# Performance work log

Hardware: AMD Instinct MI355X
Metric: run time of the kernel (lower is better)

Reference implementation:

```python
import jax, jax.numpy as jnp
import numpy as np

N_NODES = 100000
N_EDGES = 1600000
IN_DIM = 64
HID = 128
N_ASSETS = 50
N_GRAPHS = 64


def setup_inputs() -> dict:
    key = jax.random.key(0)
    ks = jax.random.split(key, 12)
    x = jax.random.normal(ks[0], (N_NODES, IN_DIM), dtype=jnp.float32)
    edge_index = jax.random.randint(ks[1], (2, N_EDGES), 0, N_NODES, dtype=jnp.int64)
    batch = jnp.sort(jax.random.randint(ks[2], (N_NODES,), 0, N_GRAPHS, dtype=jnp.int64))
    def lin(k, fan_in, fan_out):
        bound = 1.0 / np.sqrt(fan_in)
        return jax.random.uniform(k, (fan_in, fan_out), jnp.float32, -bound, bound)
    return {
        "x": x,
        "edge_index": edge_index,
        "batch": batch,
        # GraphConv 1: lin_rel (with bias) on aggregated messages, lin_root (no bias)
        "w1_rel": lin(ks[3], IN_DIM, HID),
        "b1": jnp.zeros((HID,), jnp.float32),
        "w1_root": lin(ks[4], IN_DIM, HID),
        # GraphConv 2
        "w2_rel": lin(ks[5], HID, HID),
        "b2": jnp.zeros((HID,), jnp.float32),
        "w2_root": lin(ks[6], HID, HID),
        # MLP head
        "fc1_w": lin(ks[7], HID, HID),
        "fc1_b": jnp.zeros((HID,), jnp.float32),
        "fc2_w": lin(ks[8], HID, N_ASSETS),
        "fc2_b": jnp.zeros((N_ASSETS,), jnp.float32),
    }


def graph_conv(x, src, dst, w_rel, w_root, b):
    # out_i = W_rel @ (sum_{j: j->i} x_j) + W_root @ x_i + b  (PyG GraphConv, aggr='add')
    # Project first (cheaper traffic when out_dim <= in_dim is not guaranteed, but
    # aggregating raw features then projecting matches math; project-then-scatter is
    # equivalent by linearity and lets the scatter run at out width. Keep faithful
    # order: aggregate raw x_j, then lin_rel.
    agg = jax.ops.segment_sum(x[src], dst, num_segments=N_NODES)  # [N, in_dim]
    return agg @ w_rel + x @ w_root + b


def reference(x, edge_index, batch, w1_rel, b1, w1_root, w2_rel, b2, w2_root,
              fc1_w, fc1_b, fc2_w, fc2_b):
    src, dst = edge_index[0], edge_index[1]
    h = jax.nn.relu(graph_conv(x, src, dst, w1_rel, w1_root, b1))   # [N, HID]
    h = jax.nn.relu(graph_conv(h, src, dst, w2_rel, w2_root, b2))   # [N, HID]
    # global_mean_pool over batch segment ids
    sums = jax.ops.segment_sum(h, batch, num_segments=N_GRAPHS)     # [G, HID]
    cnts = jax.ops.segment_sum(jnp.ones((h.shape[0], 1), h.dtype), batch,
                               num_segments=N_GRAPHS)               # [G, 1]
    pooled = sums / jnp.maximum(cnts, 1.0)
    out = jax.nn.relu(pooled @ fc1_w + fc1_b)
    logits = out @ fc2_w + fc2_b
    return jax.nn.softmax(logits, axis=-1)
```

## Files before the change

### kernel.cpp

```cpp
#include <hip/hip_runtime.h>
#include <math.h>

#define N_NODES_C 100000
#define N_EDGES_C 1600000
#define IN_DIM_C 64
#define HID_C 128
#define N_ASSETS_C 50
#define N_GRAPHS_C 64

#define BKT_SHIFT 9
#define BKT_NODES 512
#define NB_BKT ((N_NODES_C + BKT_NODES - 1) / BKT_NODES)
#define EPB_A 8192
#define NBLK_A ((N_EDGES_C + EPB_A - 1) / EPB_A)

typedef __attribute__((ext_vector_type(8))) short bf16x8;
typedef __attribute__((ext_vector_type(4))) float f32x4;

__device__ __forceinline__ unsigned short f2bf(float f) {
    unsigned u = __float_as_uint(f);
    return (unsigned short)((u + 0x7FFFu + ((u >> 16) & 1u)) >> 16);
}
__device__ __forceinline__ float bf2f(unsigned short b) {
    return __uint_as_float((unsigned)b << 16);
}
__device__ __forceinline__ void acc_bf8(float* acc, uint4 v) {
    acc[0] += __uint_as_float(v.x << 16);
    acc[1] += __uint_as_float(v.x & 0xFFFF0000u);
    acc[2] += __uint_as_float(v.y << 16);
    acc[3] += __uint_as_float(v.y & 0xFFFF0000u);
    acc[4] += __uint_as_float(v.z << 16);
    acc[5] += __uint_as_float(v.z & 0xFFFF0000u);
    acc[6] += __uint_as_float(v.w << 16);
    acc[7] += __uint_as_float(v.w & 0xFFFF0000u);
}

__global__ __launch_bounds__(256) void cast_bf16_kernel(
    const float* __restrict__ src, unsigned short* __restrict__ dst, int n4)
{
    int i = blockIdx.x * 256 + threadIdx.x;
    if (i < n4) {
        float4 v = ((const float4*)src)[i];
        ushort4 o;
        o.x = f2bf(v.x); o.y = f2bf(v.y); o.z = f2bf(v.z); o.w = f2bf(v.w);
        ((ushort4*)dst)[i] = o;
    }
}

__global__ __launch_bounds__(64) void pack_w_kernel(
    const float* __restrict__ W, unsigned short* __restrict__ dst)
{
    int kc = blockIdx.x >> 3;
    int ct = blockIdx.x & 7;
    int lane = threadIdx.x;
    int quad = lane >> 4;
    int l16 = lane & 15;
    unsigned short hi[8], lo[8];
#pragma unroll
    for (int j = 0; j < 8; ++j) {
        float w = W[(size_t)(kc * 32 + quad * 8 + j) * HID_C + ct * 16 + l16];
        unsigned short h = f2bf(w);
        float r = w - bf2f(h);
        hi[j] = h;
        lo[j] = f2bf(r);
    }
    size_t base = ((size_t)(kc * 8 + ct) * 2) * 512 + (size_t)lane * 8;
#pragma unroll
    for (int j = 0; j < 8; ++j) {
        dst[base + j] = hi[j];
        dst[base + 512 + j] = lo[j];
    }
}

__global__ __launch_bounds__(256) void bucket_hist_kernel(
    const int* __restrict__ ei, int* __restrict__ bcnt)
{
    __shared__ int cnt[NB_BKT];
    int t = threadIdx.x;
    for (int i = t; i < NB_BKT; i += 256) cnt[i] = 0;
    __syncthreads();
    int base = blockIdx.x * 2048;
#pragma unroll
    for (int i = 0; i < 8; ++i) {
        int e = base + i * 256 + t;
        if (e < N_EDGES_C) {
            int dst = ei[N_EDGES_C + e];
            atomicAdd(&cnt[dst >> BKT_SHIFT], 1);
        }
    }
    __syncthreads();
    for (int i = t; i < NB_BKT; i += 256)
        if (cnt[i]) atomicAdd(&bcnt[i], cnt[i]);
}

__global__ __launch_bounds__(256) void bucket_scan_kernel(
    const int* __restrict__ bcnt, int* __restrict__ bbase, int* __restrict__ gcur)
{
    __shared__ int s[256];
    int t = threadIdx.x;
    int v = (t < NB_BKT) ? bcnt[t] : 0;
    s[t] = v;
    __syncthreads();
    for (int o = 1; o < 256; o <<= 1) {
        int x = (t >= o) ? s[t - o] : 0;
        __syncthreads();
        s[t] += x;
        __syncthreads();
    }
    int excl = s[t] - v;
    if (t < NB_BKT) { bbase[t] = excl; gcur[t] = excl; }
    if (t == 255) bbase[NB_BKT] = s[255];
}

__global__ __launch_bounds__(256) void partition_kernel(
    const int* __restrict__ ei, int* __restrict__ gcur,
    unsigned* __restrict__ tmp)
{
    __shared__ unsigned stage[EPB_A];
    __shared__ unsigned stage2[EPB_A];
    __shared__ unsigned char sbkt[EPB_A];
    __shared__ unsigned char sbkt2[EPB_A];
    __shared__ int cnt[NB_BKT];
    __shared__ int base[NB_BKT];
    __shared__ int cur[NB_BKT];
    __shared__ int gb[NB_BKT];
    __shared__ int s[256];

    const int t = threadIdx.x;
    const int e0 = blockIdx.x * EPB_A;
    const int nE = min(EPB_A, N_EDGES_C - e0);

    for (int i = t; i < NB_BKT; i += 256) cnt[i] = 0;
    __syncthreads();

    for (int idx = t; idx < nE; idx += 256) {
        int e = e0 + idx;
        int src = ei[e];
        int dst = ei[N_EDGES_C + e];
        int b = dst >> BKT_SHIFT;
        stage[idx] = ((unsigned)(dst & (BKT_NODES - 1)) << 17) | (unsigned)src;
        sbkt[idx] = (unsigned char)b;
        atomicAdd(&cnt[b], 1);
    }
    __syncthreads();

    int v = (t < NB_BKT) ? cnt[t] : 0;
    s[t] = v;
    __syncthreads();
    for (int o = 1; o < 256; o <<= 1) {
        int x = (t >= o) ? s[t - o] : 0;
        __syncthreads();
        s[t] += x;
        __syncthreads();
    }
    if (t < NB_BKT) {
        int excl = s[t] - v;
        base[t] = excl;
        cur[t] = excl;
        gb[t] = atomicAdd(&gcur[t], v);
    }
    __syncthreads();

    for (int idx = t; idx < nE; idx += 256) {
        int b = sbkt[idx];
        int p = atomicAdd(&cur[b], 1);
        stage2[p] = stage[idx];
        sbkt2[p] = (unsigned char)b;
    }
    __syncthreads();

    for (int idx = t; idx < nE; idx += 256) {
        int b = sbkt2[idx];
        int dest = gb[b] + (idx - base[b]);
        tmp[dest] = stage2[idx];
    }
}

__global__ __launch_bounds__(256) void bucket_sort_kernel(
    const unsigned* __restrict__ tmp, const int* __restrict__ bbase,
    int* __restrict__ row_ptr, int* __restrict__ col)
{
    __shared__ int ldeg[BKT_NODES];
    __shared__ int lsum[256];
    const int t = threadIdx.x;
    const int b = blockIdx.x;
    const int beg = bbase[b];
    const int end = bbase[b + 1];

    ldeg[t] = 0; ldeg[t + 256] = 0;
    __syncthreads();

    for (int p = beg + t; p < end; p += 256)
        atomicAdd(&ldeg[tmp[p] >> 17], 1);
    __syncthreads();

    int a0 = ldeg[2 * t], a1 = ldeg[2 * t + 1];
    int pair = a0 + a1;
    lsum[t] = pair;
    __syncthreads();
    for (int o = 1; o < 256; o <<= 1) {
        int x = (t >= o) ? lsum[t - o] : 0;
        __syncthreads();
        lsum[t] += x;
        __syncthreads();
    }
    int ep = lsum[t] - pair;
    __syncthreads();
    ldeg[2 * t] = ep;
    ldeg[2 * t + 1] = ep + a0;

    int gn0 = b * BKT_NODES + 2 * t;
    if (gn0 < N_NODES_C)     row_ptr[gn0] = beg + ep;
    if (gn0 + 1 < N_NODES_C) row_ptr[gn0 + 1] = beg + ep + a0;
    if (b == NB_BKT - 1 && t == 0) row_ptr[N_NODES_C] = N_EDGES_C;
    __syncthreads();

    for (int p = beg + t; p < end; p += 256) {
        unsigned v = tmp[p];
        int pos = atomicAdd(&ldeg[v >> 17], 1);
        col[beg + pos] = (int)(v & 0x1FFFFu);
    }
}

__global__ __launch_bounds__(256) void gather_bf128_kernel(
    const unsigned short* __restrict__ feat, const int* __restrict__ row_ptr,
    const int* __restrict__ col, unsigned short* __restrict__ agg)
{
    int wave = threadIdx.x >> 6;
    int lane = threadIdx.x & 63;
    int g = lane >> 4;
    int c = lane & 15;
    int n = blockIdx.x * 4 + wave;
    if (n >= N_NODES_C) return;
    int beg = row_ptr[n], end = row_ptr[n + 1];
    const uint4* f4 = (const uint4*)feat;

    float acc[8];
#pragma unroll
    for (int j = 0; j < 8; ++j) acc[j] = 0.f;

    int e = beg + g;
    for (; e + 12 < end; e += 16) {
        int s0 = col[e], s1 = col[e + 4], s2 = col[e + 8], s3 = col[e + 12];
        uint4 v0 = f4[(size_t)s0 * 16 + c];
        uint4 v1 = f4[(size_t)s1 * 16 + c];
        uint4 v2 = f4[(size_t)s2 * 16 + c];
        uint4 v3 = f4[(size_t)s3 * 16 + c];
        acc_bf8(acc, v0); acc_bf8(acc, v1); acc_bf8(acc, v2); acc_bf8(acc, v3);
    }
    if (e + 4 < end) {
        int s0 = col[e], s1 = col[e + 4];
        uint4 v0 = f4[(size_t)s0 * 16 + c];
        uint4 v1 = f4[(size_t)s1 * 16 + c];
        acc_bf8(acc, v0); acc_bf8(acc, v1);
        e += 8;
    }
    if (e < end) {
        uint4 v = f4[(size_t)col[e] * 16 + c];
        acc_bf8(acc, v);
    }
#pragma unroll
    for (int j = 0; j < 8; ++j) {
        acc[j] += __shfl_xor(acc[j], 16, 64);
        acc[j] += __shfl_xor(acc[j], 32, 64);
    }
    if (g == 0) {
        uint4 o;
        o.x = (unsigned)f2bf(acc[0]) | ((unsigned)f2bf(acc[1]) << 16);
        o.y = (unsigned)f2bf(acc[2]) | ((unsigned)f2bf(acc[3]) << 16);
        o.z = (unsigned)f2bf(acc[4]) | ((unsigned)f2bf(acc[5]) << 16);
        o.w = (unsigned)f2bf(acc[6]) | ((unsigned)f2bf(acc[7]) << 16);
        ((uint4*)agg)[(size_t)n * 16 + c] = o;
    }
}

__global__ __launch_bounds__(256) void gather_bf64_kernel(
    const unsigned short* __restrict__ feat, const int* __restrict__ row_ptr,
    const int* __restrict__ col, unsigned short* __restrict__ agg)
{
    int wave = threadIdx.x >> 6;
    int lane = threadIdx.x & 63;
    int g = lane >> 3;
    int c = lane & 7;
    int n = blockIdx.x * 4 + wave;
    if (n >= N_NODES_C) return;
    int beg = row_ptr[n], end = row_ptr[n + 1];
    const uint4* f4 = (const uint4*)feat;

    float acc[8];
#pragma unroll
    for (int j = 0; j < 8; ++j) acc[j] = 0.f;

    int e = beg + g;
    for (; e + 8 < end; e += 16) {
        int s0 = col[e], s1 = col[e + 8];
        uint4 v0 = f4[(size_t)s0 * 8 + c];
        uint4 v1 = f4[(size_t)s1 * 8 + c];
        acc_bf8(acc, v0); acc_bf8(acc, v1);
    }
    if (e < end) {
        uint4 v = f4[(size_t)col[e] * 8 + c];
        acc_bf8(acc, v);
    }
#pragma unroll
    for (int j = 0; j < 8; ++j) {
        acc[j] += __shfl_xor(acc[j], 8, 64);
        acc[j] += __shfl_xor(acc[j], 16, 64);
        acc[j] += __shfl_xor(acc[j], 32, 64);
    }
    if (g == 0) {
        uint4 o;
        o.x = (unsigned)f2bf(acc[0]) | ((unsigned)f2bf(acc[1]) << 16);
        o.y = (unsigned)f2bf(acc[2]) | ((unsigned)f2bf(acc[3]) << 16);
        o.z = (unsigned)f2bf(acc[4]) | ((unsigned)f2bf(acc[5]) << 16);
        o.w = (unsigned)f2bf(acc[6]) | ((unsigned)f2bf(acc[7]) << 16);
        ((uint4*)agg)[(size_t)n * 8 + c] = o;
    }
}

template<int K>
__device__ __forceinline__ void conv_phase(
    const unsigned short* __restrict__ P, const unsigned short* __restrict__ WP,
    const int* rowIdx, int quad, int lane, int wv, f32x4 acc[4][2])
{
#pragma unroll
    for (int kc = 0; kc < K / 32; ++kc) {
        bf16x8 afr[4];
#pragma unroll
        for (int rt = 0; rt < 4; ++rt)
            afr[rt] = *(const bf16x8*)(P + (size_t)rowIdx[rt] * K + kc * 32 + quad * 8);
#pragma unroll
        for (int ci = 0; ci < 2; ++ci) {
            int ct = wv * 2 + ci;
            const unsigned short* bp = WP + ((size_t)(kc * 8 + ct) * 2) * 512 + (size_t)lane * 8;
            bf16x8 bhi = *(const bf16x8*)bp;
            bf16x8 blo = *(const bf16x8*)(bp + 512);
#pragma unroll
            for (int rt = 0; rt < 4; ++rt) {
                acc[rt][ci] = __builtin_amdgcn_mfma_f32_16x16x32_bf16(afr[rt], bhi, acc[rt][ci], 0, 0, 0);
                acc[rt][ci] = __builtin_amdgcn_mfma_f32_16x16x32_bf16(afr[rt], blo, acc[rt][ci], 0, 0, 0);
            }
        }
    }
}

template<int KA, int KX>
__global__ __launch_bounds__(256) void conv_mfma_kernel(
    const unsigned short* __restrict__ A, const unsigned short* __restrict__ X,
    const unsigned short* __restrict__ WrP, const unsigned short* __restrict__ WoP,
    const float* __restrict__ bias, unsigned short* __restrict__ outp, int N)
{
    const int t = threadIdx.x;
    const int wv = t >> 6;
    const int lane = t & 63;
    const int quad = lane >> 4;
    const int l16 = lane & 15;
    const int n0 = blockIdx.x * 64;

    f32x4 acc[4][2];
#pragma unroll
    for (int rt = 0; rt < 4; ++rt)
#pragma unroll
        for (int ci = 0; ci < 2; ++ci)
            acc[rt][ci] = (f32x4){0.f, 0.f, 0.f, 0.f};

    int rowIdx[4];
#pragma unroll
    for (int rt = 0; rt < 4; ++rt) {
        int r = n0 + rt * 16 + l16;
        rowIdx[rt] = (r < N) ? r : (N - 1);
    }

    conv_phase<KA>(A, WrP, rowIdx, quad, lane, wv, acc);
    conv_phase<KX>(X, WoP, rowIdx, quad, lane, wv, acc);

#pragma unroll
    for (int ci = 0; ci < 2; ++ci) {
        int colg = wv * 32 + ci * 16 + l16;
        float bv = bias[colg];
#pragma unroll
        for (int rt = 0; rt < 4; ++rt) {
            int nbase = n0 + rt * 16 + quad * 4;
#pragma unroll
            for (int r = 0; r < 4; ++r) {
                int node = nbase + r;
                if (node < N)
                    outp[(size_t)node * HID_C + colg] = f2bf(fmaxf(acc[rt][ci][r] + bv, 0.f));
            }
        }
    }
}

template<int KA, int KX>
__global__ __launch_bounds__(256) void conv_mfma_pool_kernel(
    const unsigned short* __restrict__ A, const unsigned short* __restrict__ X,
    const unsigned short* __restrict__ WrP, const unsigned short* __restrict__ WoP,
    const float* __restrict__ bias, const int* __restrict__ batch,
    float* __restrict__ pooled, int N)
{
    __shared__ int sbatch[64];
    const int t = threadIdx.x;
    const int wv = t >> 6;
    const int lane = t & 63;
    const int quad = lane >> 4;
    const int l16 = lane & 15;
    const int n0 = blockIdx.x * 64;

    if (t < 64) {
        int node = n0 + t;
        sbatch[t] = (node < N) ? batch[node] : -1;
    }

    f32x4 acc[4][2];
#pragma unroll
    for (int rt = 0; rt < 4; ++rt)
#pragma unroll
        for (int ci = 0; ci < 2; ++ci)
            acc[rt][ci] = (f32x4){0.f, 0.f, 0.f, 0.f};

    int rowIdx[4];
#pragma unroll
    for (int rt = 0; rt < 4; ++rt) {
        int r = n0 + rt * 16 + l16;
        rowIdx[rt] = (r < N) ? r : (N - 1);
    }

    conv_phase<KA>(A, WrP, rowIdx, quad, lane, wv, acc);
    conv_phase<KX>(X, WoP, rowIdx, quad, lane, wv, acc);
    __syncthreads();

#pragma unroll
    for (int ci = 0; ci < 2; ++ci) {
        float bv = bias[wv * 32 + ci * 16 + l16];
#pragma unroll
        for (int rt = 0; rt < 4; ++rt)
#pragma unroll
            for (int r = 0; r < 4; ++r)
                acc[rt][ci][r] = fmaxf(acc[rt][ci][r] + bv, 0.f);
    }

    int gmin = sbatch[0];
    int gmax = batch[min(n0 + 63, N - 1)];
    for (int gg = gmin; gg <= gmax; ++gg) {
#pragma unroll
        for (int ci = 0; ci < 2; ++ci) {
            float p = 0.f;
#pragma unroll
            for (int rt = 0; rt < 4; ++rt) {
                int lbase = rt * 16 + quad * 4;
#pragma unroll
                for (int r = 0; r < 4; ++r)
                    if (sbatch[lbase + r] == gg) p += acc[rt][ci][r];
            }
            p += __shfl_xor(p, 16, 64);
            p += __shfl_xor(p, 32, 64);
            if (quad == 0)
                atomicAdd(&pooled[gg * HID_C + wv * 32 + ci * 16 + l16], p);
        }
    }
}

__global__ __launch_bounds__(256) void count_kernel(
    const int* __restrict__ batch, float* __restrict__ cnts, int N)
{
    __shared__ int h[N_GRAPHS_C];
    int t = threadIdx.x;
    if (t < N_GRAPHS_C) h[t] = 0;
    __syncthreads();
    int base = (blockIdx.x * 256 + t) * 16;
    int cur = -1, c = 0;
    for (int i = 0; i < 16; ++i) {
        int n = base + i;
        if (n < N) {
            int g = batch[n];
            if (g != cur) {
                if (cur >= 0) atomicAdd(&h[cur], c);
                cur = g; c = 0;
            }
            ++c;
        }
    }
    if (cur >= 0) atomicAdd(&h[cur], c);
    __syncthreads();
    if (t < N_GRAPHS_C && h[t]) atomicAdd(&cnts[t], (float)h[t]);
}

__global__ __launch_bounds__(128) void head_kernel(
    const float* __restrict__ pooled, const float* __restrict__ cnts,
    const float* __restrict__ fc1w, const float* __restrict__ fc1b,
    const float* __restrict__ fc2w, const float* __restrict__ fc2b,
    float* __restrict__ out)
{
    __shared__ float sp[HID_C];
    __shared__ float so[HID_C];
    __shared__ float sl[64];
    __shared__ float sred[2];
    int g = blockIdx.x;
    int j = threadIdx.x;

    float inv = 1.f / fmaxf(cnts[g], 1.f);
    sp[j] = pooled[g * HID_C + j] * inv;
    __syncthreads();

    float a = fc1b[j];
    for (int k = 0; k < HID_C; ++k) a = fmaf(sp[k], fc1w[k * HID_C + j], a);
    so[j] = fmaxf(a, 0.f);
    __syncthreads();

    if (j < N_ASSETS_C) {
        float l = fc2b[j];
        for (int k = 0; k < HID_C; ++k) l = fmaf(so[k], fc2w[k * N_ASSETS_C + j], l);
        sl[j] = l;
    }
    __syncthreads();

    if (j == 0) {
        float m = -1e30f;
        for (int q = 0; q < N_ASSETS_C; ++q) m = fmaxf(m, sl[q]);
        sred[0] = m;
    }
    __syncthreads();
    if (j < N_ASSETS_C) sl[j] = expf(sl[j] - sred[0]);
    __syncthreads();
    if (j == 0) {
        float s = 0.f;
        for (int q = 0; q < N_ASSETS_C; ++q) s += sl[q];
        sred[1] = 1.f / s;
    }
    __syncthreads();
    if (j < N_ASSETS_C) out[g * N_ASSETS_C + j] = sl[j] * sred[1];
}

extern "C" void kernel_launch(void* const* d_in, const int* in_sizes, int n_in,
                              void* d_out, int out_size, void* d_ws, size_t ws_size,
                              hipStream_t stream)
{
    const float* x       = (const float*)d_in[0];
    const int*   ei      = (const int*)d_in[1];
    const int*   batch   = (const int*)d_in[2];
    const float* w1_rel  = (const float*)d_in[3];
    const float* b1      = (const float*)d_in[4];
    const float* w1_root = (const float*)d_in[5];
    const float* w2_rel  = (const float*)d_in[6];
    const float* b2      = (const float*)d_in[7];
    const float* w2_root = (const float*)d_in[8];
    const float* fc1w    = (const float*)d_in[9];
    const float* fc1b    = (const float*)d_in[10];
    const float* fc2w    = (const float*)d_in[11];
    const float* fc2b    = (const float*)d_in[12];
    float* out = (float*)d_out;

    char* ws = (char*)d_ws;
    unsigned*       tmp     = (unsigned*)(ws + 0);
    int*            col     = (int*)(ws + 6400000);
    int*            row_ptr = (int*)(ws + 12800000);
    int*            bcnt    = (int*)(ws + 13200016);
    int*            bbase   = (int*)(ws + 13200816);
    int*            gcur    = (int*)(ws + 13201616);
    unsigned short* wp1r    = (unsigned short*)(ws + 13202432);
    unsigned short* wp1o    = (unsigned short*)(ws + 13235200);
    unsigned short* wp2r    = (unsigned short*)(ws + 13267968);
    unsigned short* wp2o    = (unsigned short*)(ws + 13333504);
    float*          pooled  = (float*)(ws + 13399040);
    float*          cnts    = (float*)(ws + 13431808);
    unsigned short* xb      = (unsigned short*)(ws + 13432064);
    unsigned short* agg1b   = (unsigned short*)(ws + 26232064);
    unsigned short* h1b     = (unsigned short*)(ws + 39032064);
    unsigned short* agg2b   = (unsigned short*)(ws + 64632064);

    hipMemsetAsync(pooled, 0, 33024, stream);
    hipMemsetAsync(bcnt, 0, 800, stream);

    cast_bf16_kernel<<<(N_NODES_C * IN_DIM_C / 4 + 255) / 256, 256, 0, stream>>>(x, xb, N_NODES_C * IN_DIM_C / 4);
    pack_w_kernel<<<(IN_DIM_C / 32) * 8, 64, 0, stream>>>(w1_rel,  wp1r);
    pack_w_kernel<<<(IN_DIM_C / 32) * 8, 64, 0, stream>>>(w1_root, wp1o);
    pack_w_kernel<<<(HID_C  / 32) * 8, 64, 0, stream>>>(w2_rel,  wp2r);
    pack_w_kernel<<<(HID_C  / 32) * 8, 64, 0, stream>>>(w2_root, wp2o);

    count_kernel<<<(N_NODES_C + 4095) / 4096, 256, 0, stream>>>(batch, cnts, N_NODES_C);

    bucket_hist_kernel<<<(N_EDGES_C + 2047) / 2048, 256, 0, stream>>>(ei, bcnt);
    bucket_scan_kernel<<<1, 256, 0, stream>>>(bcnt, bbase, gcur);
    partition_kernel<<<NBLK_A, 256, 0, stream>>>(ei, gcur, tmp);
    bucket_sort_kernel<<<NB_BKT, 256, 0, stream>>>(tmp, bbase, row_ptr, col);

    const int ggrid = (N_NODES_C + 3) / 4;
    const int cgrid = (N_NODES_C + 63) / 64;

    gather_bf64_kernel<<<ggrid, 256, 0, stream>>>(xb, row_ptr, col, agg1b);
    conv_mfma_kernel<IN_DIM_C, IN_DIM_C><<<cgrid, 256, 0, stream>>>(
        agg1b, xb, wp1r, wp1o, b1, h1b, N_NODES_C);

    gather_bf128_kernel<<<ggrid, 256, 0, stream>>>(h1b, row_ptr, col, agg2b);
    conv_mfma_pool_kernel<HID_C, HID_C><<<cgrid, 256, 0, stream>>>(
        agg2b, h1b, wp2r, wp2o, b2, batch, pooled, N_NODES_C);

    head_kernel<<<N_GRAPHS_C, 128, 0, stream>>>(pooled, cnts, fc1w, fc1b, fc2w, fc2b, out);
}
```

Before: 348.2 us.

## Fuse neighbor gather into conv MFMA kernels via LDS staging, merge weight packing

Each conv kernel now gathers and sums neighbor features for its 64-node tile straight into shared memory, and the MFMA stage reads the aggregate from LDS. This removes the separate gather kernels and the global round-trip of the aggregated buffers. The four weight-pack launches are merged into one, and the two memsets are folded into one by moving bcnt next to pooled. In exchange, the gather now has less parallelism: one block covers 64 nodes sequentially, with 16 nodes per wave and the 2-way unroll used for both widths. That may hide memory latency worse than the old one-wave-per-node kernels.

```diff
diff --git a/kernel.cpp b/kernel.cpp
--- a/kernel.cpp
+++ b/kernel.cpp
@@ -34,6 +34,14 @@
     acc[6] += __uint_as_float(v.w << 16);
     acc[7] += __uint_as_float(v.w & 0xFFFF0000u);
 }
+__device__ __forceinline__ uint4 pack_bf8(const float* acc) {
+    uint4 o;
+    o.x = (unsigned)f2bf(acc[0]) | ((unsigned)f2bf(acc[1]) << 16);
+    o.y = (unsigned)f2bf(acc[2]) | ((unsigned)f2bf(acc[3]) << 16);
+    o.z = (unsigned)f2bf(acc[4]) | ((unsigned)f2bf(acc[5]) << 16);
+    o.w = (unsigned)f2bf(acc[6]) | ((unsigned)f2bf(acc[7]) << 16);
+    return o;
+}
 
 __global__ __launch_bounds__(256) void cast_bf16_kernel(
     const float* __restrict__ src, unsigned short* __restrict__ dst, int n4)
@@ -47,12 +55,11 @@
     }
 }
 
-__global__ __launch_bounds__(64) void pack_w_kernel(
-    const float* __restrict__ W, unsigned short* __restrict__ dst)
-{
-    int kc = blockIdx.x >> 3;
-    int ct = blockIdx.x & 7;
-    int lane = threadIdx.x;
+__device__ __forceinline__ void pack_w_body(
+    const float* __restrict__ W, unsigned short* __restrict__ dst, int bid, int lane)
+{
+    int kc = bid >> 3;
+    int ct = bid & 7;
     int quad = lane >> 4;
     int l16 = lane & 15;
     unsigned short hi[8], lo[8];
@@ -70,6 +77,20 @@
         dst[base + j] = hi[j];
         dst[base + 512 + j] = lo[j];
     }
+}
+
+__global__ __launch_bounds__(64) void pack_all_kernel(
+    const float* __restrict__ w1r, const float* __restrict__ w1o,
+    const float* __restrict__ w2r, const float* __restrict__ w2o,
+    unsigned short* __restrict__ p1r, unsigned short* __restrict__ p1o,
+    unsigned short* __restrict__ p2r, unsigned short* __restrict__ p2o)
+{
+    int b = blockIdx.x;
+    int lane = threadIdx.x;
+    if (b < 16)       pack_w_body(w1r, p1r, b, lane);
+    else if (b < 32)  pack_w_body(w1o, p1o, b - 16, lane);
+    else if (b < 64)  pack_w_body(w2r, p2r, b - 32, lane);
+    else              pack_w_body(w2o, p2o, b - 64, lane);
 }
 
 __global__ __launch_bounds__(256) void bucket_hist_kernel(
@@ -222,104 +243,8 @@
     }
 }
 
-__global__ __launch_bounds__(256) void gather_bf128_kernel(
-    const unsigned short* __restrict__ feat, const int* __restrict__ row_ptr,
-    const int* __restrict__ col, unsigned short* __restrict__ agg)
-{
-    int wave = threadIdx.x >> 6;
-    int lane = threadIdx.x & 63;
-    int g = lane >> 4;
-    int c = lane & 15;
-    int n = blockIdx.x * 4 + wave;
-    if (n >= N_NODES_C) return;
-    int beg = row_ptr[n], end = row_ptr[n + 1];
-    const uint4* f4 = (const uint4*)feat;
-
-    float acc[8];
-#pragma unroll
-    for (int j = 0; j < 8; ++j) acc[j] = 0.f;
-
-    int e = beg + g;
-    for (; e + 12 < end; e += 16) {
-        int s0 = col[e], s1 = col[e + 4], s2 = col[e + 8], s3 = col[e + 12];
-        uint4 v0 = f4[(size_t)s0 * 16 + c];
-        uint4 v1 = f4[(size_t)s1 * 16 + c];
-        uint4 v2 = f4[(size_t)s2 * 16 + c];
-        uint4 v3 = f4[(size_t)s3 * 16 + c];
-        acc_bf8(acc, v0); acc_bf8(acc, v1); acc_bf8(acc, v2); acc_bf8(acc, v3);
-    }
-    if (e + 4 < end) {
-        int s0 = col[e], s1 = col[e + 4];
-        uint4 v0 = f4[(size_t)s0 * 16 + c];
-        uint4 v1 = f4[(size_t)s1 * 16 + c];
-        acc_bf8(acc, v0); acc_bf8(acc, v1);
-        e += 8;
-    }
-    if (e < end) {
-        uint4 v = f4[(size_t)col[e] * 16 + c];
-        acc_bf8(acc, v);
-    }
-#pragma unroll
-    for (int j = 0; j < 8; ++j) {
-        acc[j] += __shfl_xor(acc[j], 16, 64);
-        acc[j] += __shfl_xor(acc[j], 32, 64);
-    }
-    if (g == 0) {
-        uint4 o;
-        o.x = (unsigned)f2bf(acc[0]) | ((unsigned)f2bf(acc[1]) << 16);
-        o.y = (unsigned)f2bf(acc[2]) | ((unsigned)f2bf(acc[3]) << 16);
-        o.z = (unsigned)f2bf(acc[4]) | ((unsigned)f2bf(acc[5]) << 16);
-        o.w = (unsigned)f2bf(acc[6]) | ((unsigned)f2bf(acc[7]) << 16);
-        ((uint4*)agg)[(size_t)n * 16 + c] = o;
-    }
-}
-
-__global__ __launch_bounds__(256) void gather_bf64_kernel(
-    const unsigned short* __restrict__ feat, const int* __restrict__ row_ptr,
-    const int* __restrict__ col, unsigned short* __restrict__ agg)
-{
-    int wave = threadIdx.x >> 6;
-    int lane = threadIdx.x & 63;
-    int g = lane >> 3;
-    int c = lane & 7;
-    int n = blockIdx.x * 4 + wave;
-    if (n >= N_NODES_C) return;
-    int beg = row_ptr[n], end = row_ptr[n + 1];
-    const uint4* f4 = (const uint4*)feat;
-
-    float acc[8];
-#pragma unroll
-    for (int j = 0; j < 8; ++j) acc[j] = 0.f;
-
-    int e = beg + g;
-    for (; e + 8 < end; e += 16) {
-        int s0 = col[e], s1 = col[e + 8];
-        uint4 v0 = f4[(size_t)s0 * 8 + c];
-        uint4 v1 = f4[(size_t)s1 * 8 + c];
-        acc_bf8(acc, v0); acc_bf8(acc, v1);
-    }
-    if (e < end) {
-        uint4 v = f4[(size_t)col[e] * 8 + c];
-        acc_bf8(acc, v);
-    }
-#pragma unroll
-    for (int j = 0; j < 8; ++j) {
-        acc[j] += __shfl_xor(acc[j], 8, 64);
-        acc[j] += __shfl_xor(acc[j], 16, 64);
-        acc[j] += __shfl_xor(acc[j], 32, 64);
-    }
-    if (g == 0) {
-        uint4 o;
-        o.x = (unsigned)f2bf(acc[0]) | ((unsigned)f2bf(acc[1]) << 16);
-        o.y = (unsigned)f2bf(acc[2]) | ((unsigned)f2bf(acc[3]) << 16);
-        o.z = (unsigned)f2bf(acc[4]) | ((unsigned)f2bf(acc[5]) << 16);
-        o.w = (unsigned)f2bf(acc[6]) | ((unsigned)f2bf(acc[7]) << 16);
-        ((uint4*)agg)[(size_t)n * 8 + c] = o;
-    }
-}
-
 template<int K>
-__device__ __forceinline__ void conv_phase(
+__device__ __forceinline__ void conv_phase_g(
     const unsigned short* __restrict__ P, const unsigned short* __restrict__ WP,
     const int* rowIdx, int quad, int lane, int wv, f32x4 acc[4][2])
 {
@@ -344,12 +269,46 @@
     }
 }
 
-template<int KA, int KX>
-__global__ __launch_bounds__(256) void conv_mfma_kernel(
-    const unsigned short* __restrict__ A, const unsigned short* __restrict__ X,
+template<int K, int RS>
+__device__ __forceinline__ void conv_phase_lds(
+    const unsigned short* __restrict__ sA, const unsigned short* __restrict__ WP,
+    int quad, int lane, int wv, int l16, f32x4 acc[4][2])
+{
+#pragma unroll
+    for (int kc = 0; kc < K / 32; ++kc) {
+        bf16x8 afr[4];
+#pragma unroll
+        for (int rt = 0; rt < 4; ++rt)
+            afr[rt] = *(const bf16x8*)(sA + (size_t)(rt * 16 + l16) * RS + kc * 32 + quad * 8);
+#pragma unroll
+        for (int ci = 0; ci < 2; ++ci) {
+            int ct = wv * 2 + ci;
+            const unsigned short* bp = WP + ((size_t)(kc * 8 + ct) * 2) * 512 + (size_t)lane * 8;
+            bf16x8 bhi = *(const bf16x8*)bp;
+            bf16x8 blo = *(const bf16x8*)(bp + 512);
+#pragma unroll
+            for (int rt = 0; rt < 4; ++rt) {
+                acc[rt][ci] = __builtin_amdgcn_mfma_f32_16x16x32_bf16(afr[rt], bhi, acc[rt][ci], 0, 0, 0);
+                acc[rt][ci] = __builtin_amdgcn_mfma_f32_16x16x32_bf16(afr[rt], blo, acc[rt][ci], 0, 0, 0);
+            }
+        }
+    }
+}
+
+template<int K, bool POOL>
+__global__ __launch_bounds__(256) void fused_conv_kernel(
+    const unsigned short* __restrict__ feat, const unsigned short* __restrict__ X,
+    const int* __restrict__ row_ptr, const int* __restrict__ col,
     const unsigned short* __restrict__ WrP, const unsigned short* __restrict__ WoP,
-    const float* __restrict__ bias, unsigned short* __restrict__ outp, int N)
-{
+    const float* __restrict__ bias, const int* __restrict__ batch,
+    float* __restrict__ pooled, unsigned short* __restrict__ outp, int N)
+{
+    constexpr int RS = K + 8;
+    constexpr int SG = K / 8;
+    constexpr int NSG = 64 / SG;
+    __shared__ __align__(16) unsigned short sA[64 * RS];
+    __shared__ int sbatch[64];
+
     const int t = threadIdx.x;
     const int wv = t >> 6;
     const int lane = t & 63;
@@ -357,6 +316,46 @@
     const int l16 = lane & 15;
     const int n0 = blockIdx.x * 64;
 
+    if (POOL && t < 64) {
+        int node = n0 + t;
+        sbatch[t] = (node < N) ? batch[node] : -1;
+    }
+
+    {
+        const int sg = lane / SG;
+        const int c  = lane % SG;
+        const uint4* f4 = (const uint4*)feat;
+        for (int i = 0; i < 16; ++i) {
+            int ln = wv * 16 + i;
+            int n = n0 + ln;
+            int beg = 0, end = 0;
+            if (n < N) { beg = row_ptr[n]; end = row_ptr[n + 1]; }
+            float acc[8];
+#pragma unroll
+            for (int j = 0; j < 8; ++j) acc[j] = 0.f;
+            int e = beg + sg;
+            for (; e + NSG < end; e += 2 * NSG) {
+                int s0 = col[e], s1 = col[e + NSG];
+                uint4 v0 = f4[(size_t)s0 * SG + c];
+                uint4 v1 = f4[(size_t)s1 * SG + c];
+                acc_bf8(acc, v0); acc_bf8(acc, v1);
+            }
+            if (e < end) {
+                uint4 v = f4[(size_t)col[e] * SG + c];
+                acc_bf8(acc, v);
+            }
+#pragma unroll
+            for (int j = 0; j < 8; ++j) {
+                if (NSG >= 8) acc[j] += __shfl_xor(acc[j], 8, 64);
+                acc[j] += __shfl_xor(acc[j], 16, 64);
+                acc[j] += __shfl_xor(acc[j], 32, 64);
+            }
+            if (sg == 0)
+                *(uint4*)(sA + (size_t)ln * RS + c * 8) = pack_bf8(acc);
+        }
+    }
+    __syncthreads();
+
     f32x4 acc[4][2];
 #pragma unroll
     for (int rt = 0; rt < 4; ++rt)
@@ -371,91 +370,53 @@
         rowIdx[rt] = (r < N) ? r : (N - 1);
     }
 
-    conv_phase<KA>(A, WrP, rowIdx, quad, lane, wv, acc);
-    conv_phase<KX>(X, WoP, rowIdx, quad, lane, wv, acc);
-
-#pragma unroll
-    for (int ci = 0; ci < 2; ++ci) {
-        int colg = wv * 32 + ci * 16 + l16;
-        float bv = bias[colg];
-#pragma unroll
-        for (int rt = 0; rt < 4; ++rt) {
-            int nbase = n0 + rt * 16 + quad * 4;
-#pragma unroll
-            for (int r = 0; r < 4; ++r) {
-                int node = nbase + r;
-                if (node < N)
-                    outp[(size_t)node * HID_C + colg] = f2bf(fmaxf(acc[rt][ci][r] + bv, 0.f));
-            }
-        }
-    }
-}
-
-template<int KA, int KX>
-__global__ __launch_bounds__(256) void conv_mfma_pool_kernel(
-    const unsigned short* __restrict__ A, const unsigned short* __restrict__ X,
-    const unsigned short* __restrict__ WrP, const unsigned short* __restrict__ WoP,
-    const float* __restrict__ bias, const int* __restrict__ batch,
-    float* __restrict__ pooled, int N)
-{
-    __shared__ int sbatch[64];
-    const int t = threadIdx.x;
-    const int wv = t >> 6;
-    const int lane = t & 63;
-    const int quad = lane >> 4;
-    const int l16 = lane & 15;
-    const int n0 = blockIdx.x * 64;
-
-    if (t < 64) {
-        int node = n0 + t;
-        sbatch[t] = (node < N) ? batch[node] : -1;
-    }
-
-    f32x4 acc[4][2];
-#pragma unroll
-    for (int rt = 0; rt < 4; ++rt)
-#pragma unroll
-        for (int ci = 0; ci < 2; ++ci)
-            acc[rt][ci] = (f32x4){0.f, 0.f, 0.f, 0.f};
-
-    int rowIdx[4];
-#pragma unroll
-    for (int rt = 0; rt < 4; ++rt) {
-        int r = n0 + rt * 16 + l16;
-        rowIdx[rt] = (r < N) ? r : (N - 1);
-    }
-
-    conv_phase<KA>(A, WrP, rowIdx, quad, lane, wv, acc);
-    conv_phase<KX>(X, WoP, rowIdx, quad, lane, wv, acc);
-    __syncthreads();
-
-#pragma unroll
-    for (int ci = 0; ci < 2; ++ci) {
-        float bv = bias[wv * 32 + ci * 16 + l16];
-#pragma unroll
-        for (int rt = 0; rt < 4; ++rt)
-#pragma unroll
-            for (int r = 0; r < 4; ++r)
-                acc[rt][ci][r] = fmaxf(acc[rt][ci][r] + bv, 0.f);
-    }
-
-    int gmin = sbatch[0];
-    int gmax = batch[min(n0 + 63, N - 1)];
-    for (int gg = gmin; gg <= gmax; ++gg) {
+    conv_phase_lds<K, RS>(sA, WrP, quad, lane, wv, l16, acc);
+    conv_phase_g<K>(X, WoP, rowIdx, quad, lane, wv, acc);
+
+    if (!POOL) {
 #pragma unroll
         for (int ci = 0; ci < 2; ++ci) {
-            float p = 0.f;
+            int colg = wv * 32 + ci * 16 + l16;
+            float bv = bias[colg];
 #pragma unroll
             for (int rt = 0; rt < 4; ++rt) {
-                int lbase = rt * 16 + quad * 4;
+                int nbase = n0 + rt * 16 + quad * 4;
+#pragma unroll
+                for (int r = 0; r < 4; ++r) {
+                    int node = nbase + r;
+                    if (node < N)
+                        outp[(size_t)node * HID_C + colg] = f2bf(fmaxf(acc[rt][ci][r] + bv, 0.f));
+                }
+            }
+        }
+    } else {
+#pragma unroll
+        for (int ci = 0; ci < 2; ++ci) {
+            float bv = bias[wv * 32 + ci * 16 + l16];
+#pragma unroll
+            for (int rt = 0; rt < 4; ++rt)
 #pragma unroll
                 for (int r = 0; r < 4; ++r)
-                    if (sbatch[lbase + r] == gg) p += acc[rt][ci][r];
-            }
-            p += __shfl_xor(p, 16, 64);
-            p += __shfl_xor(p, 32, 64);
-            if (quad == 0)
-                atomicAdd(&pooled[gg * HID_C + wv * 32 + ci * 16 + l16], p);
+                    acc[rt][ci][r] = fmaxf(acc[rt][ci][r] + bv, 0.f);
+        }
+        int gmin = sbatch[0];
+        int gmax = batch[min(n0 + 63, N - 1)];
+        for (int gg = gmin; gg <= gmax; ++gg) {
+#pragma unroll
+            for (int ci = 0; ci < 2; ++ci) {
+                float p = 0.f;
+#pragma unroll
+                for (int rt = 0; rt < 4; ++rt) {
+                    int lbase = rt * 16 + quad * 4;
+#pragma unroll
+                    for (int r = 0; r < 4; ++r)
+                        if (sbatch[lbase + r] == gg) p += acc[rt][ci][r];
+                }
+                p += __shfl_xor(p, 16, 64);
+                p += __shfl_xor(p, 32, 64);
+                if (quad == 0)
+                    atomicAdd(&pooled[gg * HID_C + wv * 32 + ci * 16 + l16], p);
+            }
         }
     }
 }
@@ -554,28 +515,23 @@
     unsigned*       tmp     = (unsigned*)(ws + 0);
     int*            col     = (int*)(ws + 6400000);
     int*            row_ptr = (int*)(ws + 12800000);
-    int*            bcnt    = (int*)(ws + 13200016);
-    int*            bbase   = (int*)(ws + 13200816);
-    int*            gcur    = (int*)(ws + 13201616);
-    unsigned short* wp1r    = (unsigned short*)(ws + 13202432);
-    unsigned short* wp1o    = (unsigned short*)(ws + 13235200);
-    unsigned short* wp2r    = (unsigned short*)(ws + 13267968);
-    unsigned short* wp2o    = (unsigned short*)(ws + 13333504);
-    float*          pooled  = (float*)(ws + 13399040);
-    float*          cnts    = (float*)(ws + 13431808);
-    unsigned short* xb      = (unsigned short*)(ws + 13432064);
-    unsigned short* agg1b   = (unsigned short*)(ws + 26232064);
-    unsigned short* h1b     = (unsigned short*)(ws + 39032064);
-    unsigned short* agg2b   = (unsigned short*)(ws + 64632064);
-
-    hipMemsetAsync(pooled, 0, 33024, stream);
-    hipMemsetAsync(bcnt, 0, 800, stream);
+    int*            bbase   = (int*)(ws + 13200016);
+    int*            gcur    = (int*)(ws + 13200816);
+    unsigned short* wp1r    = (unsigned short*)(ws + 13201616);
+    unsigned short* wp1o    = (unsigned short*)(ws + 13234384);
+    unsigned short* wp2r    = (unsigned short*)(ws + 13267152);
+    unsigned short* wp2o    = (unsigned short*)(ws + 13332688);
+    float*          pooled  = (float*)(ws + 13398224);
+    float*          cnts    = (float*)(ws + 13430992);
+    int*            bcnt    = (int*)(ws + 13431248);
+    unsigned short* xb      = (unsigned short*)(ws + 13432048);
+    unsigned short* h1b     = (unsigned short*)(ws + 26232048);
+
+    hipMemsetAsync(pooled, 0, 33824, stream);
 
     cast_bf16_kernel<<<(N_NODES_C * IN_DIM_C / 4 + 255) / 256, 256, 0, stream>>>(x, xb, N_NODES_C * IN_DIM_C / 4);
-    pack_w_kernel<<<(IN_DIM_C / 32) * 8, 64, 0, stream>>>(w1_rel,  wp1r);
-    pack_w_kernel<<<(IN_DIM_C / 32) * 8, 64, 0, stream>>>(w1_root, wp1o);
-    pack_w_kernel<<<(HID_C  / 32) * 8, 64, 0, stream>>>(w2_rel,  wp2r);
-    pack_w_kernel<<<(HID_C  / 32) * 8, 64, 0, stream>>>(w2_root, wp2o);
+    pack_all_kernel<<<96, 64, 0, stream>>>(w1_rel, w1_root, w2_rel, w2_root,
+                                           wp1r, wp1o, wp2r, wp2o);
 
     count_kernel<<<(N_NODES_C + 4095) / 4096, 256, 0, stream>>>(batch, cnts, N_NODES_C);
 
@@ -584,16 +540,13 @@
     partition_kernel<<<NBLK_A, 256, 0, stream>>>(ei, gcur, tmp);
     bucket_sort_kernel<<<NB_BKT, 256, 0, stream>>>(tmp, bbase, row_ptr, col);
 
-    const int ggrid = (N_NODES_C + 3) / 4;
     const int cgrid = (N_NODES_C + 63) / 64;
 
-    gather_bf64_kernel<<<ggrid, 256, 0, stream>>>(xb, row_ptr, col, agg1b);
-    conv_mfma_kernel<IN_DIM_C, IN_DIM_C><<<cgrid, 256, 0, stream>>>(
-        agg1b, xb, wp1r, wp1o, b1, h1b, N_NODES_C);
-
-    gather_bf128_kernel<<<ggrid, 256, 0, stream>>>(h1b, row_ptr, col, agg2b);
-    conv_mfma_pool_kernel<HID_C, HID_C><<<cgrid, 256, 0, stream>>>(
-        agg2b, h1b, wp2r, wp2o, b2, batch, pooled, N_NODES_C);
+    fused_conv_kernel<IN_DIM_C, false><<<cgrid, 256, 0, stream>>>(
+        xb, xb, row_ptr, col, wp1r, wp1o, b1, batch, pooled, h1b, N_NODES_C);
+
+    fused_conv_kernel<HID_C, true><<<cgrid, 256, 0, stream>>>(
+        h1b, h1b, row_ptr, col, wp2r, wp2o, b2, batch, pooled, h1b, N_NODES_C);
 
     head_kernel<<<N_GRAPHS_C, 128, 0, stream>>>(pooled, cnts, fc1w, fc1b, fc2w, fc2b, out);
 }
```

Result: slower. 389.8 us (+11.9%).

## Fuse preprocessing kernels into one launch and widen bucket sort blocks

Applied to the files above, without the earlier changes.

Merges the bf16 cast, the four weight-pack launches, the graph-count pass and the edge bucket histogram into a single preproc kernel whose block ranges pick the job. The workspace is reordered so one memset zeroes pooled, cnts and bcnt together, which drops a memset and several launches. Bucket sort now uses 512 threads per block, one node per thread, and the partition kernel handles half as many edges per block so there are more blocks. Risks are divergent block roles inside one launch and a longer scan in bucket sort.

```diff
diff --git a/kernel.cpp b/kernel.cpp
--- a/kernel.cpp
+++ b/kernel.cpp
@@ -11,8 +11,14 @@
 #define BKT_SHIFT 9
 #define BKT_NODES 512
 #define NB_BKT ((N_NODES_C + BKT_NODES - 1) / BKT_NODES)
-#define EPB_A 8192
+#define EPB_A 4096
 #define NBLK_A ((N_EDGES_C + EPB_A - 1) / EPB_A)
+
+#define PP_CAST_NB 6250
+#define PP_PACK_NB 96
+#define PP_CNT_NB 25
+#define PP_HIST_NB 782
+#define PP_NB (PP_CAST_NB + PP_PACK_NB + PP_CNT_NB + PP_HIST_NB)
 
 typedef __attribute__((ext_vector_type(8))) short bf16x8;
 typedef __attribute__((ext_vector_type(4))) float f32x4;
@@ -34,25 +40,20 @@
     acc[6] += __uint_as_float(v.w << 16);
     acc[7] += __uint_as_float(v.w & 0xFFFF0000u);
 }
-
-__global__ __launch_bounds__(256) void cast_bf16_kernel(
-    const float* __restrict__ src, unsigned short* __restrict__ dst, int n4)
-{
-    int i = blockIdx.x * 256 + threadIdx.x;
-    if (i < n4) {
-        float4 v = ((const float4*)src)[i];
-        ushort4 o;
-        o.x = f2bf(v.x); o.y = f2bf(v.y); o.z = f2bf(v.z); o.w = f2bf(v.w);
-        ((ushort4*)dst)[i] = o;
-    }
-}
-
-__global__ __launch_bounds__(64) void pack_w_kernel(
-    const float* __restrict__ W, unsigned short* __restrict__ dst)
-{
-    int kc = blockIdx.x >> 3;
-    int ct = blockIdx.x & 7;
-    int lane = threadIdx.x;
+__device__ __forceinline__ uint4 pack_bf8v(const float* acc) {
+    uint4 o;
+    o.x = (unsigned)f2bf(acc[0]) | ((unsigned)f2bf(acc[1]) << 16);
+    o.y = (unsigned)f2bf(acc[2]) | ((unsigned)f2bf(acc[3]) << 16);
+    o.z = (unsigned)f2bf(acc[4]) | ((unsigned)f2bf(acc[5]) << 16);
+    o.w = (unsigned)f2bf(acc[6]) | ((unsigned)f2bf(acc[7]) << 16);
+    return o;
+}
+
+__device__ __forceinline__ void pack_w_body(
+    const float* __restrict__ W, unsigned short* __restrict__ dst, int bid, int lane)
+{
+    int kc = bid >> 3;
+    int ct = bid & 7;
     int quad = lane >> 4;
     int l16 = lane & 15;
     unsigned short hi[8], lo[8];
@@ -72,25 +73,74 @@
     }
 }
 
-__global__ __launch_bounds__(256) void bucket_hist_kernel(
+__global__ __launch_bounds__(256) void preproc_kernel(
+    const float* __restrict__ x, unsigned short* __restrict__ xb,
+    const float* __restrict__ w1r, const float* __restrict__ w1o,
+    const float* __restrict__ w2r, const float* __restrict__ w2o,
+    unsigned short* __restrict__ p1r, unsigned short* __restrict__ p1o,
+    unsigned short* __restrict__ p2r, unsigned short* __restrict__ p2o,
+    const int* __restrict__ batch, float* __restrict__ cnts,
     const int* __restrict__ ei, int* __restrict__ bcnt)
 {
-    __shared__ int cnt[NB_BKT];
-    int t = threadIdx.x;
-    for (int i = t; i < NB_BKT; i += 256) cnt[i] = 0;
-    __syncthreads();
-    int base = blockIdx.x * 2048;
-#pragma unroll
-    for (int i = 0; i < 8; ++i) {
-        int e = base + i * 256 + t;
-        if (e < N_EDGES_C) {
-            int dst = ei[N_EDGES_C + e];
-            atomicAdd(&cnt[dst >> BKT_SHIFT], 1);
+    __shared__ int sh[NB_BKT];
+    const int b = blockIdx.x;
+    const int t = threadIdx.x;
+
+    if (b < PP_CAST_NB) {
+        int i = b * 256 + t;
+        float4 v = ((const float4*)x)[i];
+        ushort4 o;
+        o.x = f2bf(v.x); o.y = f2bf(v.y); o.z = f2bf(v.z); o.w = f2bf(v.w);
+        ((ushort4*)xb)[i] = o;
+        return;
+    }
+    if (b < PP_CAST_NB + PP_PACK_NB) {
+        if (t < 64) {
+            int pb = b - PP_CAST_NB;
+            if (pb < 16)       pack_w_body(w1r, p1r, pb, t);
+            else if (pb < 32)  pack_w_body(w1o, p1o, pb - 16, t);
+            else if (pb < 64)  pack_w_body(w2r, p2r, pb - 32, t);
+            else               pack_w_body(w2o, p2o, pb - 64, t);
         }
-    }
-    __syncthreads();
-    for (int i = t; i < NB_BKT; i += 256)
-        if (cnt[i]) atomicAdd(&bcnt[i], cnt[i]);
+        return;
+    }
+    if (b < PP_CAST_NB + PP_PACK_NB + PP_CNT_NB) {
+        if (t < N_GRAPHS_C) sh[t] = 0;
+        __syncthreads();
+        int base = ((b - PP_CAST_NB - PP_PACK_NB) * 256 + t) * 16;
+        int cur = -1, c = 0;
+        for (int i = 0; i < 16; ++i) {
+            int n = base + i;
+            if (n < N_NODES_C) {
+                int g = batch[n];
+                if (g != cur) {
+                    if (cur >= 0) atomicAdd(&sh[cur], c);
+                    cur = g; c = 0;
+                }
+                ++c;
+            }
+        }
+        if (cur >= 0) atomicAdd(&sh[cur], c);
+        __syncthreads();
+        if (t < N_GRAPHS_C && sh[t]) atomicAdd(&cnts[t], (float)sh[t]);
+        return;
+    }
+    {
+        for (int i = t; i < NB_BKT; i += 256) sh[i] = 0;
+        __syncthreads();
+        int base = (b - PP_CAST_NB - PP_PACK_NB - PP_CNT_NB) * 2048;
+#pragma unroll
+        for (int i = 0; i < 8; ++i) {
+            int e = base + i * 256 + t;
+            if (e < N_EDGES_C) {
+                int dst = ei[N_EDGES_C + e];
+                atomicAdd(&sh[dst >> BKT_SHIFT], 1);
+            }
+        }
+        __syncthreads();
+        for (int i = t; i < NB_BKT; i += 256)
+            if (sh[i]) atomicAdd(&bcnt[i], sh[i]);
+    }
 }
 
 __global__ __launch_bounds__(256) void bucket_scan_kernel(
@@ -176,49 +226,46 @@
     }
 }
 
-__global__ __launch_bounds__(256) void bucket_sort_kernel(
+__global__ __launch_bounds__(512) void bucket_sort_kernel(
     const unsigned* __restrict__ tmp, const int* __restrict__ bbase,
     int* __restrict__ row_ptr, int* __restrict__ col)
 {
     __shared__ int ldeg[BKT_NODES];
-    __shared__ int lsum[256];
+    __shared__ int lsum[512];
     const int t = threadIdx.x;
     const int b = blockIdx.x;
     const int beg = bbase[b];
     const int end = bbase[b + 1];
 
-    ldeg[t] = 0; ldeg[t + 256] = 0;
-    __syncthreads();
-
-    for (int p = beg + t; p < end; p += 256)
+    ldeg[t] = 0;
+    __syncthreads();
+
+    for (int p = beg + t; p < end; p += 512)
         atomicAdd(&ldeg[tmp[p] >> 17], 1);
     __syncthreads();
 
-    int a0 = ldeg[2 * t], a1 = ldeg[2 * t + 1];
-    int pair = a0 + a1;
-    lsum[t] = pair;
-    __syncthreads();
-    for (int o = 1; o < 256; o <<= 1) {
+    int v = ldeg[t];
+    lsum[t] = v;
+    __syncthreads();
+    for (int o = 1; o < 512; o <<= 1) {
         int x = (t >= o) ? lsum[t - o] : 0;
         __syncthreads();
         lsum[t] += x;
         __syncthreads();
     }
-    int ep = lsum[t] - pair;
-    __syncthreads();
-    ldeg[2 * t] = ep;
-    ldeg[2 * t + 1] = ep + a0;
-
-    int gn0 = b * BKT_NODES + 2 * t;
-    if (gn0 < N_NODES_C)     row_ptr[gn0] = beg + ep;
-    if (gn0 + 1 < N_NODES_C) row_ptr[gn0 + 1] = beg + ep + a0;
+    int ep = lsum[t] - v;
+    __syncthreads();
+    ldeg[t] = ep;
+
+    int gn = b * BKT_NODES + t;
+    if (gn < N_NODES_C) row_ptr[gn] = beg + ep;
     if (b == NB_BKT - 1 && t == 0) row_ptr[N_NODES_C] = N_EDGES_C;
     __syncthreads();
 
-    for (int p = beg + t; p < end; p += 256) {
-        unsigned v = tmp[p];
-        int pos = atomicAdd(&ldeg[v >> 17], 1);
-        col[beg + pos] = (int)(v & 0x1FFFFu);
+    for (int p = beg + t; p < end; p += 512) {
+        unsigned u = tmp[p];
+        int pos = atomicAdd(&ldeg[u >> 17], 1);
+        col[beg + pos] = (int)(u & 0x1FFFFu);
     }
 }
 
@@ -264,14 +311,8 @@
         acc[j] += __shfl_xor(acc[j], 16, 64);
         acc[j] += __shfl_xor(acc[j], 32, 64);
     }
-    if (g == 0) {
-        uint4 o;
-        o.x = (unsigned)f2bf(acc[0]) | ((unsigned)f2bf(acc[1]) << 16);
-        o.y = (unsigned)f2bf(acc[2]) | ((unsigned)f2bf(acc[3]) << 16);
-        o.z = (unsigned)f2bf(acc[4]) | ((unsigned)f2bf(acc[5]) << 16);
-        o.w = (unsigned)f2bf(acc[6]) | ((unsigned)f2bf(acc[7]) << 16);
-        ((uint4*)agg)[(size_t)n * 16 + c] = o;
-    }
+    if (g == 0)
+        ((uint4*)agg)[(size_t)n * 16 + c] = pack_bf8v(acc);
 }
 
 __global__ __launch_bounds__(256) void gather_bf64_kernel(
@@ -308,14 +349,8 @@
         acc[j] += __shfl_xor(acc[j], 16, 64);
         acc[j] += __shfl_xor(acc[j], 32, 64);
     }
-    if (g == 0) {
-        uint4 o;
-        o.x = (unsigned)f2bf(acc[0]) | ((unsigned)f2bf(acc[1]) << 16);
-        o.y = (unsigned)f2bf(acc[2]) | ((unsigned)f2bf(acc[3]) << 16);
-        o.z = (unsigned)f2bf(acc[4]) | ((unsigned)f2bf(acc[5]) << 16);
-        o.w = (unsigned)f2bf(acc[6]) | ((unsigned)f2bf(acc[7]) << 16);
-        ((uint4*)agg)[(size_t)n * 8 + c] = o;
-    }
+    if (g == 0)
+        ((uint4*)agg)[(size_t)n * 8 + c] = pack_bf8v(acc);
 }
 
 template<int K>
@@ -458,31 +493,6 @@
                 atomicAdd(&pooled[gg * HID_C + wv * 32 + ci * 16 + l16], p);
         }
     }
-}
-
-__global__ __launch_bounds__(256) void count_kernel(
-    const int* __restrict__ batch, float* __restrict__ cnts, int N)
-{
-    __shared__ int h[N_GRAPHS_C];
-    int t = threadIdx.x;
-    if (t < N_GRAPHS_C) h[t] = 0;
-    __syncthreads();
-    int base = (blockIdx.x * 256 + t) * 16;
-    int cur = -1, c = 0;
-    for (int i = 0; i < 16; ++i) {
-        int n = base + i;
-        if (n < N) {
-            int g = batch[n];
-            if (g != cur) {
-                if (cur >= 0) atomicAdd(&h[cur], c);
-                cur = g; c = 0;
-            }
-            ++c;
-        }
-    }
-    if (cur >= 0) atomicAdd(&h[cur], c);
-    __syncthreads();
-    if (t < N_GRAPHS_C && h[t]) atomicAdd(&cnts[t], (float)h[t]);
 }
 
 __global__ __launch_bounds__(128) void head_kernel(
@@ -554,35 +564,29 @@
     unsigned*       tmp     = (unsigned*)(ws + 0);
     int*            col     = (int*)(ws + 6400000);
     int*            row_ptr = (int*)(ws + 12800000);
-    int*            bcnt    = (int*)(ws + 13200016);
-    int*            bbase   = (int*)(ws + 13200816);
-    int*            gcur    = (int*)(ws + 13201616);
-    unsigned short* wp1r    = (unsigned short*)(ws + 13202432);
-    unsigned short* wp1o    = (unsigned short*)(ws + 13235200);
-    unsigned short* wp2r    = (unsigned short*)(ws + 13267968);
-    unsigned short* wp2o    = (unsigned short*)(ws + 13333504);
-    float*          pooled  = (float*)(ws + 13399040);
-    float*          cnts    = (float*)(ws + 13431808);
-    unsigned short* xb      = (unsigned short*)(ws + 13432064);
-    unsigned short* agg1b   = (unsigned short*)(ws + 26232064);
-    unsigned short* h1b     = (unsigned short*)(ws + 39032064);
-    unsigned short* agg2b   = (unsigned short*)(ws + 64632064);
-
-    hipMemsetAsync(pooled, 0, 33024, stream);
-    hipMemsetAsync(bcnt, 0, 800, stream);
-
-    cast_bf16_kernel<<<(N_NODES_C * IN_DIM_C / 4 + 255) / 256, 256, 0, stream>>>(x, xb, N_NODES_C * IN_DIM_C / 4);
-    pack_w_kernel<<<(IN_DIM_C / 32) * 8, 64, 0, stream>>>(w1_rel,  wp1r);
-    pack_w_kernel<<<(IN_DIM_C / 32) * 8, 64, 0, stream>>>(w1_root, wp1o);
-    pack_w_kernel<<<(HID_C  / 32) * 8, 64, 0, stream>>>(w2_rel,  wp2r);
-    pack_w_kernel<<<(HID_C  / 32) * 8, 64, 0, stream>>>(w2_root, wp2o);
-
-    count_kernel<<<(N_NODES_C + 4095) / 4096, 256, 0, stream>>>(batch, cnts, N_NODES_C);
-
-    bucket_hist_kernel<<<(N_EDGES_C + 2047) / 2048, 256, 0, stream>>>(ei, bcnt);
+    int*            bbase   = (int*)(ws + 13200016);
+    int*            gcur    = (int*)(ws + 13200816);
+    unsigned short* wp1r    = (unsigned short*)(ws + 13201616);
+    unsigned short* wp1o    = (unsigned short*)(ws + 13234384);
+    unsigned short* wp2r    = (unsigned short*)(ws + 13267152);
+    unsigned short* wp2o    = (unsigned short*)(ws + 13332688);
+    float*          pooled  = (float*)(ws + 13398224);
+    float*          cnts    = (float*)(ws + 13430992);
+    int*            bcnt    = (int*)(ws + 13431248);
+    unsigned short* xb      = (unsigned short*)(ws + 13432048);
+    unsigned short* agg1b   = (unsigned short*)(ws + 26232048);
+    unsigned short* h1b     = (unsigned short*)(ws + 39032048);
+    unsigned short* agg2b   = (unsigned short*)(ws + 64632048);
+
+    hipMemsetAsync(pooled, 0, 33824, stream);
+
+    preproc_kernel<<<PP_NB, 256, 0, stream>>>(
+        x, xb, w1_rel, w1_root, w2_rel, w2_root,
+        wp1r, wp1o, wp2r, wp2o, batch, cnts, ei, bcnt);
+
     bucket_scan_kernel<<<1, 256, 0, stream>>>(bcnt, bbase, gcur);
     partition_kernel<<<NBLK_A, 256, 0, stream>>>(ei, gcur, tmp);
-    bucket_sort_kernel<<<NB_BKT, 256, 0, stream>>>(tmp, bbase, row_ptr, col);
+    bucket_sort_kernel<<<NB_BKT, 512, 0, stream>>>(tmp, bbase, row_ptr, col);
 
     const int ggrid = (N_NODES_C + 3) / 4;
     const int cgrid = (N_NODES_C + 63) / 64;
```

Measured after the change: 357.3 us. 1.03x slower.
